# Optimization experiments

Hardware: AMD Instinct MI355X
Metric: run time of the kernel (lower is better)

The kernel has to match this reference:

```python
import jax, jax.numpy as jnp
import numpy as np


def _skew_relative(QE):
    # QE: [B, H, N, 2N-1] -> [B, H, N, N] relative-position skew (Music-Transformer style)
    B, H, N, L = QE.shape  # L == 2N - 1
    x = jnp.pad(QE, ((0, 0), (0, 0), (0, 0), (0, 1))).reshape(B, H, N * (L + 1))
    x = jnp.pad(x, ((0, 0), (0, 0), (0, N - 1))).reshape(B, H, N + 1, 2 * N - 1)
    return x[:, :, :N, -N:]


def setup_inputs() -> dict:
    key = jax.random.key(0)
    ks = jax.random.split(key, 8)
    B, N, D, H, dh = 8, 1024, 512, 8, 64
    W_SCALE = 0.02
    return {
        "x": jax.random.normal(ks[0], (B, N, D), jnp.float32),
        "phase": jax.random.uniform(ks[1], (B, H, N, 1), jnp.float32),
        "E_rel": jax.random.normal(ks[2], (2 * N - 1, dh), jnp.float32) * 0.05,
        "W_q": jax.random.normal(ks[3], (H * dh, D), jnp.float32) * W_SCALE,
        "W_k": jax.random.normal(ks[4], (H * dh, D), jnp.float32) * W_SCALE,
        "W_v": jax.random.normal(ks[5], (H * dh, D), jnp.float32) * W_SCALE,
        "W_o": jax.random.normal(ks[6], (D, H * dh), jnp.float32) * W_SCALE,
        "b_o": jnp.zeros((D,), jnp.float32),
    }


def reference(x, phase, E_rel, W_q, W_k, W_v, W_o, b_o):
    B, N, _ = x.shape
    H = phase.shape[1]
    dh = W_q.shape[0] // H
    scale = 1.0 / (dh ** 0.5)

    def heads(W):  # [B,N,H*dh] -> [B,H,N,dh]
        return (x @ W.T).reshape(B, N, H, dh).transpose(0, 2, 1, 3)

    Q, K, V = heads(W_q), heads(W_k), heads(W_v)
    attn = jnp.einsum('bhnd,bhmd->bhnm', Q, K)
    attn = attn + _skew_relative(jnp.einsum('bhnd,ld->bhnl', Q, E_rel))
    attn = jax.nn.softmax(attn * scale, axis=-1)
    out = jnp.einsum('bhnm,bhmd->bhnd', attn, V) * phase  # phase-modulated AV
    out = out.transpose(0, 2, 1, 3).reshape(B, N, H * dh)
    return out @ W_o.T + b_o  # dropout is identity in eval mode
```

## Files before the change

### kernel.cpp

```cpp
#include <hip/hip_runtime.h>


typedef __bf16 bf16x8 __attribute__((ext_vector_type(8)));
typedef __bf16 bf16x4 __attribute__((ext_vector_type(4)));
typedef float  f32x4  __attribute__((ext_vector_type(4)));
typedef float  f32x16 __attribute__((ext_vector_type(16)));

#if __has_builtin(__builtin_amdgcn_exp2f)
#define EXP2(x) __builtin_amdgcn_exp2f(x)
#else
#define EXP2(x) exp2f(x)
#endif

#define QSCALE 0.18033688011f

#define GLOAD_LDS16(g, l)                                                      \
    __builtin_amdgcn_global_load_lds(                                          \
        (const __attribute__((address_space(1))) unsigned int*)(g),            \
        (__attribute__((address_space(3))) unsigned int*)(l), 16, 0, 0)


__global__ __launch_bounds__(256) void cvt_all(const float* __restrict__ x,
                                               const float* __restrict__ E,
                                               const float* __restrict__ wq,
                                               const float* __restrict__ wk,
                                               const float* __restrict__ wv,
                                               const float* __restrict__ wo,
                                               __bf16* __restrict__ xb,
                                               __bf16* __restrict__ Ef,
                                               __bf16* __restrict__ wqkv,
                                               __bf16* __restrict__ wob) {
    int i = blockIdx.x * 256 + threadIdx.x;
    if (i >= 1081328 ? i < 1343472 : i < 1048576) {
        const float* s; __bf16* d; int off;
        if      (i < 1048576) { s = x;  d = xb;            off = i; }
        else if (i < 1146864) { s = wq; d = wqkv;          off = i - 1081328; }
        else if (i < 1212400) { s = wk; d = wqkv + 262144; off = i - 1146864; }
        else if (i < 1277936) { s = wv; d = wqkv + 524288; off = i - 1212400; }
        else                  { s = wo; d = wob;           off = i - 1277936; }
        float4 v = *(const float4*)(s + (size_t)off * 4);
        bf16x4 o;
        o[0] = (__bf16)v.x; o[1] = (__bf16)v.y; o[2] = (__bf16)v.z; o[3] = (__bf16)v.w;
        *(bf16x4*)(d + (size_t)off * 4) = o;
    } else if (i >= 1048576 && i < 1081328) {
        int off = i - 1048576;
        float4 v = *(const float4*)(E + (size_t)off * 4);
        int e0i = off * 4;
        int l = e0i >> 6, d0 = e0i & 63;
        int t32 = l >> 5, cq = l & 31, ks = d0 >> 4, hf = (d0 >> 3) & 1, j = d0 & 7;
        bf16x4 o;
        o[0] = (__bf16)v.x; o[1] = (__bf16)v.y; o[2] = (__bf16)v.z; o[3] = (__bf16)v.w;
        *(bf16x4*)(Ef + ((size_t)((t32 * 4 + ks) * 64) + hf * 32 + cq) * 8 + j) = o;
    }
}

__global__ __launch_bounds__(256) void gemm_qkv(const __bf16* __restrict__ X,
                                                const __bf16* __restrict__ W,
                                                __bf16* __restrict__ Qb,
                                                __bf16* __restrict__ Kf,
                                                __bf16* __restrict__ Vf) {
    __shared__ __bf16 Xs[128][64];
    __shared__ __bf16 Ws[128][64];
    const int tid = threadIdx.x;
    const int wave = tid >> 6, lane = tid & 63;
    const int col = lane & 15, quad = lane >> 4;
    const int m_base = blockIdx.x * 128;
    const int j_base = blockIdx.y * 128;
    const bool qk = (j_base < 1024);
    const int wm = (wave & 1) * 64;
    const int wn = (wave >> 1) * 64;
    const f32x4 fz = {0.f, 0.f, 0.f, 0.f};
    f32x4 acc[4][4];
#pragma unroll
    for (int i = 0; i < 4; ++i)
#pragma unroll
        for (int j = 0; j < 4; ++j) acc[i][j] = fz;

    for (int k0 = 0; k0 < 512; k0 += 64) {
#pragma unroll
        for (int p = 0; p < 4; ++p) {
            int s = tid + p * 256;
            int row = s >> 3, cc = (s & 7) * 8;
            GLOAD_LDS16(X + (size_t)(m_base + row) * 512 + k0 + cc, &Xs[0][0] + (size_t)s * 8);
            GLOAD_LDS16(W + (size_t)(j_base + row) * 512 + k0 + cc, &Ws[0][0] + (size_t)s * 8);
        }
        __syncthreads();
#pragma unroll
        for (int kk = 0; kk < 64; kk += 32) {
            bf16x8 xa[4], wb[4];
#pragma unroll
            for (int i = 0; i < 4; ++i) xa[i] = *(const bf16x8*)(&Xs[wm + i * 16 + col][kk + quad * 8]);
#pragma unroll
            for (int j = 0; j < 4; ++j) wb[j] = *(const bf16x8*)(&Ws[wn + j * 16 + col][kk + quad * 8]);
            if (qk) {
#pragma unroll
                for (int i = 0; i < 4; ++i)
#pragma unroll
                    for (int j = 0; j < 4; ++j)
                        acc[i][j] = __builtin_amdgcn_mfma_f32_16x16x32_bf16(wb[i], xa[j], acc[i][j], 0, 0, 0);
            } else {
#pragma unroll
                for (int i = 0; i < 4; ++i)
#pragma unroll
                    for (int j = 0; j < 4; ++j)
                        acc[i][j] = __builtin_amdgcn_mfma_f32_16x16x32_bf16(xa[i], wb[j], acc[i][j], 0, 0, 0);
            }
        }
        __syncthreads();
    }
    if (qk) {
#pragma unroll
        for (int i = 0; i < 4; ++i) {
#pragma unroll
            for (int j = 0; j < 4; ++j) {
                int jabs = j_base + wn + i * 16 + quad * 4;
                int m = m_base + wm + j * 16 + col;
                int b_ = m >> 10, n = m & 1023;
                int rem = jabs & 511, h = rem >> 6, d = rem & 63;
                bf16x4 v;
                if (jabs < 512) {
                    v[0] = (__bf16)(acc[i][j][0] * QSCALE);
                    v[1] = (__bf16)(acc[i][j][1] * QSCALE);
                    v[2] = (__bf16)(acc[i][j][2] * QSCALE);
                    v[3] = (__bf16)(acc[i][j][3] * QSCALE);
                    *(bf16x4*)(Qb + (((size_t)b_ * 8 + h) * 1024 + n) * 64 + d) = v;
                } else {
                    v[0] = (__bf16)acc[i][j][0]; v[1] = (__bf16)acc[i][j][1];
                    v[2] = (__bf16)acc[i][j][2]; v[3] = (__bf16)acc[i][j][3];
                    int t32 = n >> 5, cq = n & 31, ks = d >> 4, hf = (d >> 3) & 1, jj = d & 7;
                    *(bf16x4*)(Kf + (size_t)(b_ * 8 + h) * 65536 +
                               ((size_t)((t32 * 4 + ks) * 64) + hf * 32 + cq) * 8 + jj) = v;
                }
            }
        }
    } else {
#pragma unroll
        for (int i = 0; i < 4; ++i) {
#pragma unroll
            for (int j = 0; j < 4; ++j) {
                int m = m_base + wm + i * 16 + quad * 4;
                int b_ = m >> 10, n = m & 1023;
                int jabs = j_base + wn + j * 16 + col;
                int rem = jabs & 511, h = rem >> 6, d = rem & 63;
                int t64 = n >> 6, ks = (n >> 4) & 3, hf = (n >> 3) & 1, jj = n & 7;
                int dhalf = d >> 5, cq = d & 31;
                bf16x4 v;
                v[0] = (__bf16)acc[i][j][0]; v[1] = (__bf16)acc[i][j][1];
                v[2] = (__bf16)acc[i][j][2]; v[3] = (__bf16)acc[i][j][3];
                *(bf16x4*)(Vf + (size_t)(b_ * 8 + h) * 65536 +
                           ((size_t)(((t64 * 4 + ks) * 2 + dhalf) * 64) + hf * 32 + cq) * 8 + jj) = v;
            }
        }
    }
}

#define FLASH_HALF(T, KC0, KC1, KN0, KN1)                                              \
  {                                                                                    \
    const int t_ = (T);                                                                \
    const int teB_ = te0 + 2 * t_ + 1;                                                 \
    bf16x8 e1f[4], e2f[4], v0f[4], v1f[4];                                             \
    _Pragma("unroll")                                                                  \
    for (int ks = 0; ks < 4; ++ks) {                                                   \
      e1f[ks] = *(const bf16x8*)(Ef + ((size_t)((teB_ * 4 + ks) * 64) + lane) * 8);    \
      e2f[ks] = *(const bf16x8*)(Ef + ((size_t)(((teB_ + 1) * 4 + ks) * 64) + lane) * 8); \
    }                                                                                  \
    _Pragma("unroll")                                                                  \
    for (int ks = 0; ks < 4; ++ks) {                                                   \
      v0f[ks] = *(const bf16x8*)(Vfb + ((size_t)(((t_ * 4 + ks) * 2 + 0) * 64) + lane) * 8); \
      v1f[ks] = *(const bf16x8*)(Vfb + ((size_t)(((t_ * 4 + ks) * 2 + 1) * 64) + lane) * 8); \
    }                                                                                  \
    f32x16 qeB = z16, qeC = z16, s0 = z16, s1 = z16;                                   \
    _Pragma("unroll")                                                                  \
    for (int ks = 0; ks < 4; ++ks) {                                                   \
      s0 = __builtin_amdgcn_mfma_f32_32x32x16_bf16(a_q[ks], KC0[ks], s0, 0, 0, 0);     \
      s1 = __builtin_amdgcn_mfma_f32_32x32x16_bf16(a_q[ks], KC1[ks], s1, 0, 0, 0);     \
    }                                                                                  \
    const int t32n_ = (((T) + 1) & 15) * 2;                                            \
    _Pragma("unroll")                                                                  \
    for (int ks = 0; ks < 4; ++ks) {                                                   \
      KN0[ks] = *(const bf16x8*)(Kfb + ((size_t)((t32n_ * 4 + ks) * 64) + lane) * 8);  \
      KN1[ks] = *(const bf16x8*)(Kfb + ((size_t)(((t32n_ + 1) * 4 + ks) * 64) + lane) * 8); \
    }                                                                                  \
    _Pragma("unroll")                                                                  \
    for (int ks = 0; ks < 4; ++ks) {                                                   \
      qeB = __builtin_amdgcn_mfma_f32_32x32x16_bf16(a_q[ks], e1f[ks], qeB, 0, 0, 0);   \
      qeC = __builtin_amdgcn_mfma_f32_32x32x16_bf16(a_q[ks], e2f[ks], qeC, 0, 0, 0);   \
    }                                                                                  \
    _Pragma("unroll")                                                                  \
    for (int r = 0; r < 16; ++r) {                                                     \
      int row = (r & 3) + 8 * (r >> 2) + 4 * half;                                     \
      int tt = colq + 31 - row;                                                        \
      int src = (tt & 31) | (half << 5);                                               \
      float shB = __shfl(qeB[r], src, 64);                                             \
      float shC = __shfl(qeC[r], src, 64);                                             \
      bool sel = (tt >= 32);                                                           \
      float rel0 = sel ? shB : shA[r];                                                 \
      float rel1 = sel ? shC : shB;                                                    \
      float p0 = EXP2(s0[r] + rel0);                                                   \
      float p1 = EXP2(s1[r] + rel1);                                                   \
      rowsum[r] += p0 + p1;                                                            \
      Pw[w][row][colq]      = (__bf16)p0;                                              \
      Pw[w][row][32 + colq] = (__bf16)p1;                                              \
      shA[r] = shC;                                                                    \
    }                                                                                  \
    asm volatile("s_waitcnt lgkmcnt(0)" ::: "memory");                                 \
    _Pragma("unroll")                                                                  \
    for (int ks = 0; ks < 4; ++ks) {                                                   \
      bf16x8 pa = *(const bf16x8*)(&Pw[w][colq][ks * 16 + half * 8]);                  \
      o0 = __builtin_amdgcn_mfma_f32_32x32x16_bf16(pa, v0f[ks], o0, 0, 0, 0);          \
      o1 = __builtin_amdgcn_mfma_f32_32x32x16_bf16(pa, v1f[ks], o1, 0, 0, 0);          \
    }                                                                                  \
    asm volatile("" ::: "memory");                                                     \
  }

__global__ __launch_bounds__(128, 2) void flash_kernel(const __bf16* __restrict__ Qb,
                                                       const __bf16* __restrict__ Kf,
                                                       const __bf16* __restrict__ Vf,
                                                       const __bf16* __restrict__ Ef,
                                                       const float* __restrict__ phase,
                                                       __bf16* __restrict__ Ob) {
    const int wg = blockIdx.x;
    const int xcd = wg & 7;
    const int slot = wg >> 3;
    const int bh = xcd * 8 + (slot >> 4);
    const int n0 = (slot & 15) * 64;
    const int w = threadIdx.x >> 6, lane = threadIdx.x & 63;
    const int colq = lane & 31, half = lane >> 5;
    const int nbase = n0 + w * 32;

    __shared__ __bf16 Pw[2][32][72];

    f32x16 z16;
#pragma unroll
    for (int i = 0; i < 16; ++i) z16[i] = 0.f;

    bf16x8 a_q[4];
#pragma unroll
    for (int ks = 0; ks < 4; ++ks)
        a_q[ks] = *(const bf16x8*)(Qb + ((size_t)bh * 1024 + nbase + colq) * 64 + ks * 16 + half * 8);

    f32x16 o0 = z16, o1 = z16;
    float rowsum[16];
#pragma unroll
    for (int i = 0; i < 16; ++i) rowsum[i] = 0.f;

    const __bf16* Kfb = Kf + (size_t)bh * 65536;
    const __bf16* Vfb = Vf + (size_t)bh * 65536;

    const int te0 = (992 - nbase) >> 5;

    bf16x8 kA0[4], kA1[4], kB0[4], kB1[4];
#pragma unroll
    for (int ks = 0; ks < 4; ++ks) {
        kA0[ks] = *(const bf16x8*)(Kfb + ((size_t)((0 * 4 + ks) * 64) + lane) * 8);
        kA1[ks] = *(const bf16x8*)(Kfb + ((size_t)((1 * 4 + ks) * 64) + lane) * 8);
    }

    float shA[16];
    {
        f32x16 qeA = z16;
#pragma unroll
        for (int ks = 0; ks < 4; ++ks) {
            bf16x8 e = *(const bf16x8*)(Ef + ((size_t)((te0 * 4 + ks) * 64) + lane) * 8);
            qeA = __builtin_amdgcn_mfma_f32_32x32x16_bf16(a_q[ks], e, qeA, 0, 0, 0);
        }
#pragma unroll
        for (int r = 0; r < 16; ++r) {
            int row = (r & 3) + 8 * (r >> 2) + 4 * half;
            int tt = colq + 31 - row;
            int src = (tt & 31) | (half << 5);
            shA[r] = __shfl(qeA[r], src, 64);
        }
    }

#pragma unroll 1
    for (int tt2 = 0; tt2 < 8; ++tt2) {
        FLASH_HALF(2 * tt2,     kA0, kA1, kB0, kB1)
        FLASH_HALF(2 * tt2 + 1, kB0, kB1, kA0, kA1)
    }

    const int b_ = bh >> 3, hh = bh & 7;
#pragma unroll
    for (int r = 0; r < 16; ++r) {
        float l = rowsum[r];
        l += __shfl_xor(l, 1, 32);
        l += __shfl_xor(l, 2, 32);
        l += __shfl_xor(l, 4, 32);
        l += __shfl_xor(l, 8, 32);
        l += __shfl_xor(l, 16, 32);
        int row = (r & 3) + 8 * (r >> 2) + 4 * half;
        float f = phase[(size_t)bh * 1024 + nbase + row] / l;
        Pw[w][row][colq]      = (__bf16)(o0[r] * f);
        Pw[w][row][32 + colq] = (__bf16)(o1[r] * f);
    }
    asm volatile("s_waitcnt lgkmcnt(0)" ::: "memory");
    {
        int row = lane >> 1, dseg = lane & 1;
        bf16x8 u0 = *(const bf16x8*)(&Pw[w][row][dseg * 32]);
        bf16x8 u1 = *(const bf16x8*)(&Pw[w][row][dseg * 32 + 8]);
        bf16x8 u2 = *(const bf16x8*)(&Pw[w][row][dseg * 32 + 16]);
        bf16x8 u3 = *(const bf16x8*)(&Pw[w][row][dseg * 32 + 24]);
        size_t obase = ((size_t)b_ * 1024 + nbase + row) * 512 + hh * 64 + dseg * 32;
        *(bf16x8*)(Ob + obase)      = u0;
        *(bf16x8*)(Ob + obase + 8)  = u1;
        *(bf16x8*)(Ob + obase + 16) = u2;
        *(bf16x8*)(Ob + obase + 24) = u3;
    }
}

__global__ __launch_bounds__(256) void gemm_out(const __bf16* __restrict__ X,
                                                const __bf16* __restrict__ W,
                                                const float* __restrict__ bo,
                                                float* __restrict__ out) {
    __shared__ __bf16 Xs[128][64];
    __shared__ __bf16 Ws[64][64];
    const int tid = threadIdx.x;
    const int wave = tid >> 6, lane = tid & 63;
    const int col = lane & 15, quad = lane >> 4;
    const int m_base = blockIdx.x * 128;
    const int j_base = blockIdx.y * 64;
    const int wm = (wave & 1) * 64;
    const int wn = (wave >> 1) * 32;
    const f32x4 fz = {0.f, 0.f, 0.f, 0.f};
    f32x4 acc[2][4];
#pragma unroll
    for (int i = 0; i < 2; ++i)
#pragma unroll
        for (int j = 0; j < 4; ++j) acc[i][j] = fz;

    for (int k0 = 0; k0 < 512; k0 += 64) {
#pragma unroll
        for (int p = 0; p < 4; ++p) {
            int s = tid + p * 256;
            int row = s >> 3, cc = (s & 7) * 8;
            GLOAD_LDS16(X + (size_t)(m_base + row) * 512 + k0 + cc, &Xs[0][0] + (size_t)s * 8);
        }
#pragma unroll
        for (int p = 0; p < 2; ++p) {
            int s = tid + p * 256;
            int row = s >> 3, cc = (s & 7) * 8;
            GLOAD_LDS16(W + (size_t)(j_base + row) * 512 + k0 + cc, &Ws[0][0] + (size_t)s * 8);
        }
        __syncthreads();
#pragma unroll
        for (int kk = 0; kk < 64; kk += 32) {
            bf16x8 xa[4], wb[2];
#pragma unroll
            for (int j = 0; j < 4; ++j) xa[j] = *(const bf16x8*)(&Xs[wm + j * 16 + col][kk + quad * 8]);
#pragma unroll
            for (int i = 0; i < 2; ++i) wb[i] = *(const bf16x8*)(&Ws[wn + i * 16 + col][kk + quad * 8]);
#pragma unroll
            for (int i = 0; i < 2; ++i)
#pragma unroll
                for (int j = 0; j < 4; ++j)
                    acc[i][j] = __builtin_amdgcn_mfma_f32_16x16x32_bf16(wb[i], xa[j], acc[i][j], 0, 0, 0);
        }
        __syncthreads();
    }
#pragma unroll
    for (int i = 0; i < 2; ++i) {
#pragma unroll
        for (int j = 0; j < 4; ++j) {
            int jabs = j_base + wn + i * 16 + quad * 4;
            int m = m_base + wm + j * 16 + col;
            f32x4 bv = *(const f32x4*)(bo + jabs);
            f32x4 o = acc[i][j] + bv;
            *(f32x4*)(out + (size_t)m * 512 + jabs) = o;
        }
    }
}

extern "C" void kernel_launch(void* const* d_in, const int* in_sizes, int n_in,
                              void* d_out, int out_size, void* d_ws, size_t ws_size,
                              hipStream_t stream) {
    (void)in_sizes; (void)n_in; (void)out_size; (void)ws_size;
    const float* x     = (const float*)d_in[0];
    const float* phase = (const float*)d_in[1];
    const float* E_rel = (const float*)d_in[2];
    const float* W_q   = (const float*)d_in[3];
    const float* W_k   = (const float*)d_in[4];
    const float* W_v   = (const float*)d_in[5];
    const float* W_o   = (const float*)d_in[6];
    const float* b_o   = (const float*)d_in[7];
    float* out = (float*)d_out;

    char* ws = (char*)d_ws;
    __bf16* xb   = (__bf16*)(ws);
    __bf16* wqkv = (__bf16*)(ws + 8388608);
    __bf16* wob  = (__bf16*)(ws + 9961472);
    __bf16* Ef   = (__bf16*)(ws + 10485760);
    __bf16* Qb   = (__bf16*)(ws + 10747904);
    __bf16* Kf   = (__bf16*)(ws + 19136512);
    __bf16* Vf   = (__bf16*)(ws + 27525120);
    __bf16* Ob   = (__bf16*)(ws + 35913728);

    cvt_all<<<dim3(5249), dim3(256), 0, stream>>>(x, E_rel, W_q, W_k, W_v, W_o,
                                                  xb, Ef, wqkv, wob);
    gemm_qkv<<<dim3(64, 12), dim3(256), 0, stream>>>(xb, wqkv, Qb, Kf, Vf);
    flash_kernel<<<dim3(1024), dim3(128), 0, stream>>>(Qb, Kf, Vf, Ef, phase, Ob);
    gemm_out<<<dim3(64, 8), dim3(256), 0, stream>>>(Ob, wob, b_o, out);
}
```

Before: 171.1 us.

## Split key range across the two waves of each flash workgroup and combine in LDS

Each workgroup now covers 32 query rows instead of 64. Its two waves each process half of the key/relative-position tiles, and wave 1's partial outputs and row sums are merged into wave 0 through shared memory before the normalized write. The grid doubles to 2048 workgroups and the launch bound allows 4 blocks per CU, which exposes more parallelism and shortens each wave's serial loop. The cost is extra LDS traffic, a block barrier, duplicated Q loads per wave, and possible register pressure or spills from the tighter occupancy bound.

```diff
diff --git a/kernel.cpp b/kernel.cpp
--- a/kernel.cpp
+++ b/kernel.cpp
@@ -213,7 +213,7 @@
     asm volatile("" ::: "memory");                                                     \
   }
 
-__global__ __launch_bounds__(128, 2) void flash_kernel(const __bf16* __restrict__ Qb,
+__global__ __launch_bounds__(128, 4) void flash_kernel(const __bf16* __restrict__ Qb,
                                                        const __bf16* __restrict__ Kf,
                                                        const __bf16* __restrict__ Vf,
                                                        const __bf16* __restrict__ Ef,
@@ -222,13 +222,15 @@
     const int wg = blockIdx.x;
     const int xcd = wg & 7;
     const int slot = wg >> 3;
-    const int bh = xcd * 8 + (slot >> 4);
-    const int n0 = (slot & 15) * 64;
+    const int bh = xcd * 8 + (slot >> 5);
+    const int nbase = (slot & 31) * 32;
     const int w = threadIdx.x >> 6, lane = threadIdx.x & 63;
     const int colq = lane & 31, half = lane >> 5;
-    const int nbase = n0 + w * 32;
+    const int tstart = w * 8;
 
     __shared__ __bf16 Pw[2][32][72];
+    __shared__ float Osum[32][64];
+    __shared__ float Lsum[32];
 
     f32x16 z16;
 #pragma unroll
@@ -248,12 +250,13 @@
     const __bf16* Vfb = Vf + (size_t)bh * 65536;
 
     const int te0 = (992 - nbase) >> 5;
+    const int teP = te0 + 2 * tstart;
 
     bf16x8 kA0[4], kA1[4], kB0[4], kB1[4];
 #pragma unroll
     for (int ks = 0; ks < 4; ++ks) {
-        kA0[ks] = *(const bf16x8*)(Kfb + ((size_t)((0 * 4 + ks) * 64) + lane) * 8);
-        kA1[ks] = *(const bf16x8*)(Kfb + ((size_t)((1 * 4 + ks) * 64) + lane) * 8);
+        kA0[ks] = *(const bf16x8*)(Kfb + ((size_t)(((2 * tstart) * 4 + ks) * 64) + lane) * 8);
+        kA1[ks] = *(const bf16x8*)(Kfb + ((size_t)(((2 * tstart + 1) * 4 + ks) * 64) + lane) * 8);
     }
 
     float shA[16];
@@ -261,7 +264,7 @@
         f32x16 qeA = z16;
 #pragma unroll
         for (int ks = 0; ks < 4; ++ks) {
-            bf16x8 e = *(const bf16x8*)(Ef + ((size_t)((te0 * 4 + ks) * 64) + lane) * 8);
+            bf16x8 e = *(const bf16x8*)(Ef + ((size_t)((teP * 4 + ks) * 64) + lane) * 8);
             qeA = __builtin_amdgcn_mfma_f32_32x32x16_bf16(a_q[ks], e, qeA, 0, 0, 0);
         }
 #pragma unroll
@@ -274,12 +277,11 @@
     }
 
 #pragma unroll 1
-    for (int tt2 = 0; tt2 < 8; ++tt2) {
-        FLASH_HALF(2 * tt2,     kA0, kA1, kB0, kB1)
-        FLASH_HALF(2 * tt2 + 1, kB0, kB1, kA0, kA1)
-    }
-
-    const int b_ = bh >> 3, hh = bh & 7;
+    for (int tt2 = 0; tt2 < 4; ++tt2) {
+        FLASH_HALF(tstart + 2 * tt2,     kA0, kA1, kB0, kB1)
+        FLASH_HALF(tstart + 2 * tt2 + 1, kB0, kB1, kA0, kA1)
+    }
+
 #pragma unroll
     for (int r = 0; r < 16; ++r) {
         float l = rowsum[r];
@@ -288,23 +290,44 @@
         l += __shfl_xor(l, 4, 32);
         l += __shfl_xor(l, 8, 32);
         l += __shfl_xor(l, 16, 32);
-        int row = (r & 3) + 8 * (r >> 2) + 4 * half;
-        float f = phase[(size_t)bh * 1024 + nbase + row] / l;
-        Pw[w][row][colq]      = (__bf16)(o0[r] * f);
-        Pw[w][row][32 + colq] = (__bf16)(o1[r] * f);
-    }
-    asm volatile("s_waitcnt lgkmcnt(0)" ::: "memory");
-    {
-        int row = lane >> 1, dseg = lane & 1;
-        bf16x8 u0 = *(const bf16x8*)(&Pw[w][row][dseg * 32]);
-        bf16x8 u1 = *(const bf16x8*)(&Pw[w][row][dseg * 32 + 8]);
-        bf16x8 u2 = *(const bf16x8*)(&Pw[w][row][dseg * 32 + 16]);
-        bf16x8 u3 = *(const bf16x8*)(&Pw[w][row][dseg * 32 + 24]);
-        size_t obase = ((size_t)b_ * 1024 + nbase + row) * 512 + hh * 64 + dseg * 32;
-        *(bf16x8*)(Ob + obase)      = u0;
-        *(bf16x8*)(Ob + obase + 8)  = u1;
-        *(bf16x8*)(Ob + obase + 16) = u2;
-        *(bf16x8*)(Ob + obase + 24) = u3;
+        rowsum[r] = l;
+    }
+
+    if (w == 1) {
+#pragma unroll
+        for (int r = 0; r < 16; ++r) {
+            int row = (r & 3) + 8 * (r >> 2) + 4 * half;
+            Osum[row][colq]      = o0[r];
+            Osum[row][32 + colq] = o1[r];
+            if (colq == 0) Lsum[row] = rowsum[r];
+        }
+    }
+    __syncthreads();
+    if (w == 0) {
+        const int b_ = bh >> 3, hh = bh & 7;
+#pragma unroll
+        for (int r = 0; r < 16; ++r) {
+            int row = (r & 3) + 8 * (r >> 2) + 4 * half;
+            float l = rowsum[r] + Lsum[row];
+            float f = phase[(size_t)bh * 1024 + nbase + row] / l;
+            float a0 = o0[r] + Osum[row][colq];
+            float a1 = o1[r] + Osum[row][32 + colq];
+            Pw[0][row][colq]      = (__bf16)(a0 * f);
+            Pw[0][row][32 + colq] = (__bf16)(a1 * f);
+        }
+        asm volatile("s_waitcnt lgkmcnt(0)" ::: "memory");
+        {
+            int row = lane >> 1, dseg = lane & 1;
+            bf16x8 u0 = *(const bf16x8*)(&Pw[0][row][dseg * 32]);
+            bf16x8 u1 = *(const bf16x8*)(&Pw[0][row][dseg * 32 + 8]);
+            bf16x8 u2 = *(const bf16x8*)(&Pw[0][row][dseg * 32 + 16]);
+            bf16x8 u3 = *(const bf16x8*)(&Pw[0][row][dseg * 32 + 24]);
+            size_t obase = ((size_t)b_ * 1024 + nbase + row) * 512 + hh * 64 + dseg * 32;
+            *(bf16x8*)(Ob + obase)      = u0;
+            *(bf16x8*)(Ob + obase + 8)  = u1;
+            *(bf16x8*)(Ob + obase + 16) = u2;
+            *(bf16x8*)(Ob + obase + 24) = u3;
+        }
     }
 }
 
@@ -397,6 +420,6 @@
     cvt_all<<<dim3(5249), dim3(256), 0, stream>>>(x, E_rel, W_q, W_k, W_v, W_o,
                                                   xb, Ef, wqkv, wob);
     gemm_qkv<<<dim3(64, 12), dim3(256), 0, stream>>>(xb, wqkv, Qb, Kf, Vf);
-    flash_kernel<<<dim3(1024), dim3(128), 0, stream>>>(Qb, Kf, Vf, Ef, phase, Ob);
+    flash_kernel<<<dim3(2048), dim3(128), 0, stream>>>(Qb, Kf, Vf, Ef, phase, Ob);
     gemm_out<<<dim3(64, 8), dim3(256), 0, stream>>>(Ob, wob, b_o, out);
 }
```

Result: slower. 571.3 us (+233.8%).
